# Kernel tuning notes

Measured on AMD Instinct MI355X. Metric: run time of the kernel, lower is better.

The kernel has to match this reference:

```python
import jax, jax.numpy as jnp
import numpy as np

N_NODES = 50000
N_EDGES = 600000
N_FEAT = 128
NHID = 128
N_CLASSES = 10
N_GRAPHS = 512
BN_EPS = 1e-5


def _gcn_conv(x, W, b, src, dst, n):
    """PyG GCNConv: D^{-1/2}(A+I)D^{-1/2} X W + b (symmetric norm, self-loops)."""
    xw = x @ W  # [n, out]
    deg = jax.ops.segment_sum(jnp.ones(src.shape[0], x.dtype), dst, num_segments=n) + 1.0
    dinv = jax.lax.rsqrt(deg)  # [n]
    norm = dinv[src] * dinv[dst]  # [E]
    agg = jax.ops.segment_sum(xw[src] * norm[:, None], dst, num_segments=n)
    agg = agg + xw * (dinv * dinv)[:, None]  # self-loop contribution
    return agg + b


def setup_inputs() -> dict:
    key = jax.random.key(0)
    ks = jax.random.split(key, 16)
    s_in = 1.0 / np.sqrt(N_FEAT)
    s_h = 1.0 / np.sqrt(NHID)
    s_h2 = 1.0 / np.sqrt(NHID // 2)
    return {
        "x": jax.random.normal(ks[0], (N_NODES, N_FEAT), jnp.float32),
        "edge_index": jax.random.randint(ks[1], (2, N_EDGES), 0, N_NODES, jnp.int32),
        "batch": jnp.sort(jax.random.randint(ks[2], (N_NODES,), 0, N_GRAPHS, jnp.int32)),
        "W1": jax.random.normal(ks[3], (N_FEAT, NHID), jnp.float32) * s_in,
        "b1": jnp.zeros((NHID,), jnp.float32),
        "W2": jax.random.normal(ks[4], (NHID, NHID), jnp.float32) * s_h,
        "b2": jnp.zeros((NHID,), jnp.float32),
        "W3": jax.random.normal(ks[5], (NHID, NHID), jnp.float32) * s_h,
        "b3": jnp.zeros((NHID,), jnp.float32),
        "gamma": jnp.ones((NHID,), jnp.float32),
        "beta": jnp.zeros((NHID,), jnp.float32),
        "run_mean": jnp.zeros((NHID,), jnp.float32),
        "run_var": jnp.ones((NHID,), jnp.float32),
        "lw1": jax.random.normal(ks[6], (NHID, NHID), jnp.float32) * s_h,
        "lb1": jnp.zeros((NHID,), jnp.float32),
        "lw2": jax.random.normal(ks[7], (NHID, NHID // 2), jnp.float32) * s_h,
        "lb2": jnp.zeros((NHID // 2,), jnp.float32),
        "lw3": jax.random.normal(ks[8], (NHID // 2, N_CLASSES), jnp.float32) * s_h2,
        "lb3": jnp.zeros((N_CLASSES,), jnp.float32),
    }


def reference(x, edge_index, batch, W1, b1, W2, b2, W3, b3,
              gamma, beta, run_mean, run_var,
              lw1, lb1, lw2, lb2, lw3, lb3):
    src, dst = edge_index[0], edge_index[1]
    h = jax.nn.relu(_gcn_conv(x, W1, b1, src, dst, N_NODES))
    h = jax.nn.relu(_gcn_conv(h, W2, b2, src, dst, N_NODES))
    h = jax.nn.relu(_gcn_conv(h, W3, b3, src, dst, N_NODES))
    # BatchNorm1d (eval: running stats)
    h = (h - run_mean) * jax.lax.rsqrt(run_var + BN_EPS) * gamma + beta
    # scatter_max over graph ids -> [N_GRAPHS, NHID]
    g = jax.ops.segment_max(h, batch, num_segments=N_GRAPHS)
    g = jax.nn.relu(g @ lw1 + lb1)
    g = jax.nn.relu(g @ lw2 + lb2)
    return g @ lw3 + lb3
```

## Files before the change

### kernel.cpp

```cpp
#include <hip/hip_runtime.h>
#include <hip/hip_bf16.h>

#define NHID 128
#define NGRAPH 512
#define NCLS 10

typedef __attribute__((ext_vector_type(8))) short bf16x8;
typedef __attribute__((ext_vector_type(4))) float f32x4;
typedef __attribute__((ext_vector_type(4))) unsigned int u32x4;

__device__ inline unsigned int fenc(float f) {
    unsigned int u = __float_as_uint(f);
    return (u & 0x80000000u) ? ~u : (u | 0x80000000u);
}
__device__ inline float fdec(unsigned int u) {
    u = (u & 0x80000000u) ? (u & 0x7fffffffu) : ~u;
    return __uint_as_float(u);
}
__device__ inline unsigned short f2bf(float f) {
    unsigned int u = __float_as_uint(f);
    return (unsigned short)((u + 0x7fffu + ((u >> 16) & 1u)) >> 16);
}
__device__ inline unsigned int packbf(float lo, float hi) {
    return (unsigned)f2bf(lo) | ((unsigned)f2bf(hi) << 16);
}

__global__ void k_front(const int* __restrict__ dst, int* __restrict__ cnt, int E, int degB,
                        const float* __restrict__ x, unsigned int* __restrict__ xb, int n8, int xB,
                        const float* __restrict__ W1, const float* __restrict__ W2,
                        const float* __restrict__ W3, unsigned short* __restrict__ Wt,
                        unsigned int* __restrict__ keys) {
    int b = blockIdx.x;
    if (b < degB) {
        int e = b * 256 + threadIdx.x;
        if (e < E) atomicAdd(&cnt[dst[e]], 1);
    } else if (b < degB + xB) {
        int i = (b - degB) * 256 + threadIdx.x;
        if (i < n8) {
            const float* p = x + (size_t)i * 8;
            f32x4 a = *reinterpret_cast<const f32x4*>(p);
            f32x4 c = *reinterpret_cast<const f32x4*>(p + 4);
            u32x4 o;
            o[0] = packbf(a[0], a[1]);
            o[1] = packbf(a[2], a[3]);
            o[2] = packbf(c[0], c[1]);
            o[3] = packbf(c[2], c[3]);
            *reinterpret_cast<u32x4*>(xb + (size_t)i * 4) = o;
        }
    } else if (b < degB + xB + 192) {
        int idx = (b - degB - xB) * 256 + threadIdx.x;
        int l = idx >> 14;
        int r = idx & 16383;
        const float* W = (l == 0) ? W1 : (l == 1) ? W2 : W3;
        int c = r & 127, k = r >> 7;
        Wt[l * 16384 + c * NHID + k] = f2bf(W[k * NHID + c]);
    } else {
        int i = (b - degB - xB - 192) * 256 + threadIdx.x;
        if (i < NGRAPH * NHID) keys[i] = 0u;
    }
}

__global__ __launch_bounds__(1024) void k_scan1(const int* __restrict__ cnt,
        float* __restrict__ dinv, int* __restrict__ rowptr,
        int* __restrict__ bsum, int N) {
    __shared__ int lds[1024];
    int t = threadIdx.x;
    int i = blockIdx.x * 1024 + t;
    int v = (i < N) ? cnt[i] : 0;
    if (i < N) dinv[i] = rsqrtf((float)v + 1.0f);
    lds[t] = v;
    __syncthreads();
    for (int off = 1; off < 1024; off <<= 1) {
        int x = (t >= off) ? lds[t - off] : 0;
        __syncthreads();
        lds[t] += x;
        __syncthreads();
    }
    if (i < N) rowptr[i] = lds[t] - v;
    if (t == 1023) bsum[blockIdx.x] = lds[1023];
}

__global__ __launch_bounds__(1024) void k_scan2(int* __restrict__ bsum, int nb) {
    __shared__ int lds[1024];
    int t = threadIdx.x;
    int v = (t < nb) ? bsum[t] : 0;
    lds[t] = v;
    __syncthreads();
    for (int off = 1; off < 1024; off <<= 1) {
        int x = (t >= off) ? lds[t - off] : 0;
        __syncthreads();
        lds[t] += x;
        __syncthreads();
    }
    if (t < nb) bsum[t] = lds[t] - v;
}

__global__ void k_fill(const int* __restrict__ src, const int* __restrict__ dst,
                       const int* __restrict__ rowptr, const int* __restrict__ bsum,
                       int* __restrict__ cursor, int* __restrict__ csr_src, int E) {
    int e = blockIdx.x * blockDim.x + threadIdx.x;
    if (e >= E) return;
    int s = src[e], d = dst[e];
    int pos = rowptr[d] + bsum[d >> 10] + atomicAdd(&cursor[d], 1);
    csr_src[pos] = s;
}

__device__ inline void fma8(const u32x4& u, float nw, float* a) {
#pragma unroll
    for (int q = 0; q < 4; ++q) {
        a[2 * q]     = fmaf(nw, __uint_as_float(u[q] << 16), a[2 * q]);
        a[2 * q + 1] = fmaf(nw, __uint_as_float(u[q] & 0xffff0000u), a[2 * q + 1]);
    }
}

__device__ inline void gather_row(const unsigned int* __restrict__ Hin,
        const int* __restrict__ csr_src, const int* __restrict__ rowptr,
        const int* __restrict__ bsum, const int* __restrict__ cnt,
        const float* __restrict__ dinv, unsigned int (*lds)[68],
        int w, int wv, int g, int l16, int N) {
    if (w < N) {
        float diw = dinv[w];
        u32x4 us = reinterpret_cast<const u32x4*>(Hin + (size_t)w * (NHID / 2))[l16];
        float a[8];
#pragma unroll
        for (int e = 0; e < 8; ++e) a[e] = 0.f;
        int beg = rowptr[w] + bsum[w >> 10];
        int deg = cnt[w];
        int end = beg + deg;
        int trips = (deg + 15) >> 4;
        int j = beg + g;
        for (int t = 0; t < trips; ++t, j += 16) {
            int s0 = w, s1 = w, s2 = w, s3 = w;
            if (j < end)      s0 = csr_src[j];
            if (j + 4 < end)  s1 = csr_src[j + 4];
            if (j + 8 < end)  s2 = csr_src[j + 8];
            if (j + 12 < end) s3 = csr_src[j + 12];
            float n0 = (j < end)      ? dinv[s0] * diw : 0.f;
            float n1 = (j + 4 < end)  ? dinv[s1] * diw : 0.f;
            float n2 = (j + 8 < end)  ? dinv[s2] * diw : 0.f;
            float n3 = (j + 12 < end) ? dinv[s3] * diw : 0.f;
            u32x4 u0 = reinterpret_cast<const u32x4*>(Hin + (size_t)s0 * (NHID / 2))[l16];
            u32x4 u1 = reinterpret_cast<const u32x4*>(Hin + (size_t)s1 * (NHID / 2))[l16];
            u32x4 u2 = reinterpret_cast<const u32x4*>(Hin + (size_t)s2 * (NHID / 2))[l16];
            u32x4 u3 = reinterpret_cast<const u32x4*>(Hin + (size_t)s3 * (NHID / 2))[l16];
            fma8(u0, n0, a);
            fma8(u1, n1, a);
            fma8(u2, n2, a);
            fma8(u3, n3, a);
        }
        if (g == 0) fma8(us, diw * diw, a);
#pragma unroll
        for (int e = 0; e < 8; ++e) {
            a[e] += __shfl_xor(a[e], 16);
            a[e] += __shfl_xor(a[e], 32);
        }
        if (g == 0) {
            u32x4 o;
            o[0] = packbf(a[0], a[1]);
            o[1] = packbf(a[2], a[3]);
            o[2] = packbf(a[4], a[5]);
            o[3] = packbf(a[6], a[7]);
            *reinterpret_cast<u32x4*>(&lds[wv][l16 * 4]) = o;
        }
    } else if (g == 0) {
        u32x4 z = {0u, 0u, 0u, 0u};
        *reinterpret_cast<u32x4*>(&lds[wv][l16 * 4]) = z;
    }
}

__global__ __launch_bounds__(1024) void k_agg_gemm(const unsigned int* __restrict__ Hin,
        const int* __restrict__ csr_src, const int* __restrict__ rowptr,
        const int* __restrict__ bsum, const int* __restrict__ cnt,
        const float* __restrict__ dinv, const unsigned short* __restrict__ Wt,
        const float* __restrict__ bias, unsigned short* __restrict__ Hout, int N) {
    __shared__ unsigned int lds[16][68];
    int wv = threadIdx.x >> 6;
    int lane = threadIdx.x & 63;
    int g = lane >> 4;
    int l16 = lane & 15;
    int w = blockIdx.x * 16 + wv;
    gather_row(Hin, csr_src, rowptr, bsum, cnt, dinv, lds, w, wv, g, l16, N);
    __syncthreads();
    if (wv < 8) {
        int lr = l16;
        int kq = g;
        f32x4 acc = {0.f, 0.f, 0.f, 0.f};
#pragma unroll
        for (int kg = 0; kg < 4; ++kg) {
            bf16x8 af = *reinterpret_cast<const bf16x8*>(&lds[lr][kg * 16 + kq * 4]);
            bf16x8 bf = *reinterpret_cast<const bf16x8*>(
                Wt + (size_t)(wv * 16 + lr) * NHID + kg * 32 + kq * 8);
            acc = __builtin_amdgcn_mfma_f32_16x16x32_bf16(af, bf, acc, 0, 0, 0);
        }
        int c = wv * 16 + lr;
        float b = bias[c];
#pragma unroll
        for (int e = 0; e < 4; ++e) {
            int r = blockIdx.x * 16 + kq * 4 + e;
            if (r < N) {
                float v = fmaxf(acc[e] + b, 0.f);
                Hout[(size_t)r * NHID + c] = f2bf(v);
            }
        }
    }
}

__global__ __launch_bounds__(1024) void k_agg_gemm_bn(const unsigned int* __restrict__ Hin,
        const int* __restrict__ csr_src, const int* __restrict__ rowptr,
        const int* __restrict__ bsum, const int* __restrict__ cnt,
        const float* __restrict__ dinv, const unsigned short* __restrict__ Wt,
        const float* __restrict__ bias, const int* __restrict__ batch,
        const float* __restrict__ gamma, const float* __restrict__ beta,
        const float* __restrict__ rmean, const float* __restrict__ rvar,
        unsigned int* __restrict__ keys, int N) {
    __shared__ unsigned int lds[16][68];
    __shared__ unsigned int smax[16][NHID];
    __shared__ int bseg[16];
    int tid = threadIdx.x;
    int wv = tid >> 6;
    int lane = tid & 63;
    int g = lane >> 4;
    int l16 = lane & 15;
    int n0 = blockIdx.x * 16;
    for (int i = tid; i < 16 * NHID; i += 1024) ((unsigned int*)smax)[i] = 0u;
    if (tid < 16) {
        int r = n0 + tid;
        bseg[tid] = batch[r < N ? r : N - 1];
    }
    int w = n0 + wv;
    gather_row(Hin, csr_src, rowptr, bsum, cnt, dinv, lds, w, wv, g, l16, N);
    __syncthreads();
    if (wv < 8) {
        int lr = l16;
        int kq = g;
        f32x4 acc = {0.f, 0.f, 0.f, 0.f};
#pragma unroll
        for (int kg = 0; kg < 4; ++kg) {
            bf16x8 af = *reinterpret_cast<const bf16x8*>(&lds[lr][kg * 16 + kq * 4]);
            bf16x8 bf = *reinterpret_cast<const bf16x8*>(
                Wt + (size_t)(wv * 16 + lr) * NHID + kg * 32 + kq * 8);
            acc = __builtin_amdgcn_mfma_f32_16x16x32_bf16(af, bf, acc, 0, 0, 0);
        }
        int c = wv * 16 + lr;
        float b = bias[c];
        float sc = gamma[c] * rsqrtf(rvar[c] + 1e-5f);
        float sh = beta[c] - rmean[c] * sc;
        int glo = bseg[0];
#pragma unroll
        for (int e = 0; e < 4; ++e) {
            int rr = kq * 4 + e;
            if (n0 + rr < N) {
                float v = fmaxf(acc[e] + b, 0.f);
                float y = fmaf(v, sc, sh);
                atomicMax(&smax[bseg[rr] - glo][c], fenc(y));
            }
        }
    }
    __syncthreads();
    int glo = bseg[0];
    int last = N - 1 - n0;
    if (last > 15) last = 15;
    int span = bseg[last] - glo + 1;
    for (int i = tid; i < span * NHID; i += 1024) {
        unsigned int v = ((unsigned int*)smax)[i];
        if (v) atomicMax(&keys[(size_t)(glo + (i >> 7)) * NHID + (i & 127)], v);
    }
}

__global__ __launch_bounds__(128) void k_head(const unsigned int* __restrict__ keys,
        const float* __restrict__ lw1, const float* __restrict__ lb1,
        const float* __restrict__ lw2, const float* __restrict__ lb2,
        const float* __restrict__ lw3, const float* __restrict__ lb3,
        float* __restrict__ out) {
    __shared__ float g0[NHID], g1[NHID], g2[64];
    int r = blockIdx.x;
    int t = threadIdx.x;
    unsigned int u = keys[(size_t)r * NHID + t];
    g0[t] = (u == 0u) ? -3.0e38f : fdec(u);
    __syncthreads();
    float acc = lb1[t];
#pragma unroll 8
    for (int k = 0; k < NHID; ++k) acc = fmaf(g0[k], lw1[k * NHID + t], acc);
    g1[t] = fmaxf(acc, 0.f);
    __syncthreads();
    if (t < 64) {
        acc = lb2[t];
#pragma unroll 8
        for (int k = 0; k < NHID; ++k) acc = fmaf(g1[k], lw2[k * 64 + t], acc);
        g2[t] = fmaxf(acc, 0.f);
    }
    __syncthreads();
    if (t < NCLS) {
        acc = lb3[t];
#pragma unroll 8
        for (int k = 0; k < 64; ++k) acc = fmaf(g2[k], lw3[k * NCLS + t], acc);
        out[(size_t)r * NCLS + t] = acc;
    }
}

extern "C" void kernel_launch(void* const* d_in, const int* in_sizes, int n_in,
                              void* d_out, int out_size, void* d_ws, size_t ws_size,
                              hipStream_t stream) {
    const float* x     = (const float*)d_in[0];
    const int*   ei    = (const int*)d_in[1];
    const int*   batch = (const int*)d_in[2];
    const float* W1 = (const float*)d_in[3];
    const float* b1 = (const float*)d_in[4];
    const float* W2 = (const float*)d_in[5];
    const float* b2 = (const float*)d_in[6];
    const float* W3 = (const float*)d_in[7];
    const float* b3 = (const float*)d_in[8];
    const float* gamma = (const float*)d_in[9];
    const float* beta  = (const float*)d_in[10];
    const float* rmean = (const float*)d_in[11];
    const float* rvar  = (const float*)d_in[12];
    const float* lw1 = (const float*)d_in[13];
    const float* lb1 = (const float*)d_in[14];
    const float* lw2 = (const float*)d_in[15];
    const float* lb2 = (const float*)d_in[16];
    const float* lw3 = (const float*)d_in[17];
    const float* lb3 = (const float*)d_in[18];

    const int N = in_sizes[2];
    const int E = in_sizes[1] / 2;
    const int* src = ei;
    const int* dst = ei + E;

    char* ws = (char*)d_ws;
    size_t off = 0;
    auto alloc = [&](size_t bytes) {
        char* p = ws + off;
        off += (bytes + 255) & ~(size_t)255;
        return p;
    };
    int*   cnt     = (int*)  alloc((size_t)N * 8);
    int*   cursor  = cnt + N;
    int*   rowptr  = (int*)  alloc((size_t)N * 4);
    int*   bsum    = (int*)  alloc(1024 * 4);
    float* dinv    = (float*)alloc((size_t)N * 4);
    int*   csr_src = (int*)  alloc((size_t)E * 4);
    unsigned int* xb   = (unsigned int*)alloc((size_t)N * NHID * 2);
    unsigned int* Hb   = (unsigned int*)alloc((size_t)N * NHID * 2);
    unsigned int* H2   = (unsigned int*)alloc((size_t)N * NHID * 2);
    unsigned short* Wt = (unsigned short*)alloc((size_t)3 * NHID * NHID * 2);
    unsigned int* keys = (unsigned int*)alloc((size_t)NGRAPH * NHID * 4);
    (void)ws_size; (void)n_in; (void)out_size;

    hipMemsetAsync(cnt, 0, (size_t)N * 8, stream);

    int degB = (E + 255) / 256;
    int n8 = N * 16;
    int xB = (n8 + 255) / 256;
    int frontB = degB + xB + 192 + (NGRAPH * NHID + 255) / 256;
    k_front<<<frontB, 256, 0, stream>>>(dst, cnt, E, degB, x, xb, n8, xB,
                                        W1, W2, W3, Wt, keys);
    int nb1 = (N + 1023) / 1024;
    k_scan1<<<nb1, 1024, 0, stream>>>(cnt, dinv, rowptr, bsum, N);
    k_scan2<<<1, 1024, 0, stream>>>(bsum, nb1);
    k_fill<<<degB, 256, 0, stream>>>(src, dst, rowptr, bsum, cursor, csr_src, E);

    int fgb = (N + 15) / 16;
    k_agg_gemm<<<fgb, 1024, 0, stream>>>(xb, csr_src, rowptr, bsum, cnt, dinv,
                                         Wt, b1, (unsigned short*)Hb, N);
    k_agg_gemm<<<fgb, 1024, 0, stream>>>(Hb, csr_src, rowptr, bsum, cnt, dinv,
                                         Wt + 16384, b2, (unsigned short*)H2, N);
    k_agg_gemm_bn<<<fgb, 1024, 0, stream>>>(H2, csr_src, rowptr, bsum, cnt, dinv,
                                            Wt + 32768, b3, batch, gamma, beta,
                                            rmean, rvar, keys, N);

    k_head<<<NGRAPH, 128, 0, stream>>>(keys, lw1, lb1, lw2, lb2, lw3, lb3, (float*)d_out);
}
```

Baseline: 234.0 us.

## Process 32 rows per block so all 16 waves run MFMA after gather

Measured after the change: 232.3 us, median of 2. No clear change (-0.7%).

```diff
diff --git a/kernel.cpp b/kernel.cpp
--- a/kernel.cpp
+++ b/kernel.cpp
@@ -117,7 +117,7 @@
         const int* __restrict__ csr_src, const int* __restrict__ rowptr,
         const int* __restrict__ bsum, const int* __restrict__ cnt,
         const float* __restrict__ dinv, unsigned int (*lds)[68],
-        int w, int wv, int g, int l16, int N) {
+        int w, int row, int g, int l16, int N) {
     if (w < N) {
         float diw = dinv[w];
         u32x4 us = reinterpret_cast<const u32x4*>(Hin + (size_t)w * (NHID / 2))[l16];
@@ -160,11 +160,11 @@
             o[1] = packbf(a[2], a[3]);
             o[2] = packbf(a[4], a[5]);
             o[3] = packbf(a[6], a[7]);
-            *reinterpret_cast<u32x4*>(&lds[wv][l16 * 4]) = o;
+            *reinterpret_cast<u32x4*>(&lds[row][l16 * 4]) = o;
         }
     } else if (g == 0) {
         u32x4 z = {0u, 0u, 0u, 0u};
-        *reinterpret_cast<u32x4*>(&lds[wv][l16 * 4]) = z;
+        *reinterpret_cast<u32x4*>(&lds[row][l16 * 4]) = z;
     }
 }
 
@@ -173,34 +173,36 @@
         const int* __restrict__ bsum, const int* __restrict__ cnt,
         const float* __restrict__ dinv, const unsigned short* __restrict__ Wt,
         const float* __restrict__ bias, unsigned short* __restrict__ Hout, int N) {
-    __shared__ unsigned int lds[16][68];
+    __shared__ unsigned int lds[32][68];
     int wv = threadIdx.x >> 6;
     int lane = threadIdx.x & 63;
     int g = lane >> 4;
     int l16 = lane & 15;
-    int w = blockIdx.x * 16 + wv;
-    gather_row(Hin, csr_src, rowptr, bsum, cnt, dinv, lds, w, wv, g, l16, N);
-    __syncthreads();
-    if (wv < 8) {
-        int lr = l16;
-        int kq = g;
-        f32x4 acc = {0.f, 0.f, 0.f, 0.f};
-#pragma unroll
-        for (int kg = 0; kg < 4; ++kg) {
-            bf16x8 af = *reinterpret_cast<const bf16x8*>(&lds[lr][kg * 16 + kq * 4]);
-            bf16x8 bf = *reinterpret_cast<const bf16x8*>(
-                Wt + (size_t)(wv * 16 + lr) * NHID + kg * 32 + kq * 8);
-            acc = __builtin_amdgcn_mfma_f32_16x16x32_bf16(af, bf, acc, 0, 0, 0);
-        }
-        int c = wv * 16 + lr;
-        float b = bias[c];
-#pragma unroll
-        for (int e = 0; e < 4; ++e) {
-            int r = blockIdx.x * 16 + kq * 4 + e;
-            if (r < N) {
-                float v = fmaxf(acc[e] + b, 0.f);
-                Hout[(size_t)r * NHID + c] = f2bf(v);
-            }
+    int n0 = blockIdx.x * 32;
+    gather_row(Hin, csr_src, rowptr, bsum, cnt, dinv, lds, n0 + 2 * wv,     2 * wv,     g, l16, N);
+    gather_row(Hin, csr_src, rowptr, bsum, cnt, dinv, lds, n0 + 2 * wv + 1, 2 * wv + 1, g, l16, N);
+    __syncthreads();
+    int rh = wv >> 3;
+    int ct = wv & 7;
+    int lr = l16;
+    int kq = g;
+    f32x4 acc = {0.f, 0.f, 0.f, 0.f};
+#pragma unroll
+    for (int kg = 0; kg < 4; ++kg) {
+        bf16x8 af = *reinterpret_cast<const bf16x8*>(&lds[rh * 16 + lr][kg * 16 + kq * 4]);
+        bf16x8 bf = *reinterpret_cast<const bf16x8*>(
+            Wt + (size_t)(ct * 16 + lr) * NHID + kg * 32 + kq * 8);
+        acc = __builtin_amdgcn_mfma_f32_16x16x32_bf16(af, bf, acc, 0, 0, 0);
+    }
+    int c = ct * 16 + lr;
+    float b = bias[c];
+#pragma unroll
+    for (int e = 0; e < 4; ++e) {
+        int rr = rh * 16 + kq * 4 + e;
+        int r = n0 + rr;
+        if (r < N) {
+            float v = fmaxf(acc[e] + b, 0.f);
+            Hout[(size_t)r * NHID + c] = f2bf(v);
         }
     }
 }
@@ -213,53 +215,52 @@
         const float* __restrict__ gamma, const float* __restrict__ beta,
         const float* __restrict__ rmean, const float* __restrict__ rvar,
         unsigned int* __restrict__ keys, int N) {
-    __shared__ unsigned int lds[16][68];
-    __shared__ unsigned int smax[16][NHID];
-    __shared__ int bseg[16];
+    __shared__ unsigned int lds[32][68];
+    __shared__ unsigned int smax[32][NHID];
+    __shared__ int bseg[32];
     int tid = threadIdx.x;
     int wv = tid >> 6;
     int lane = tid & 63;
     int g = lane >> 4;
     int l16 = lane & 15;
-    int n0 = blockIdx.x * 16;
-    for (int i = tid; i < 16 * NHID; i += 1024) ((unsigned int*)smax)[i] = 0u;
-    if (tid < 16) {
+    int n0 = blockIdx.x * 32;
+    for (int i = tid; i < 32 * NHID; i += 1024) ((unsigned int*)smax)[i] = 0u;
+    if (tid < 32) {
         int r = n0 + tid;
         bseg[tid] = batch[r < N ? r : N - 1];
     }
-    int w = n0 + wv;
-    gather_row(Hin, csr_src, rowptr, bsum, cnt, dinv, lds, w, wv, g, l16, N);
-    __syncthreads();
-    if (wv < 8) {
-        int lr = l16;
-        int kq = g;
-        f32x4 acc = {0.f, 0.f, 0.f, 0.f};
-#pragma unroll
-        for (int kg = 0; kg < 4; ++kg) {
-            bf16x8 af = *reinterpret_cast<const bf16x8*>(&lds[lr][kg * 16 + kq * 4]);
-            bf16x8 bf = *reinterpret_cast<const bf16x8*>(
-                Wt + (size_t)(wv * 16 + lr) * NHID + kg * 32 + kq * 8);
-            acc = __builtin_amdgcn_mfma_f32_16x16x32_bf16(af, bf, acc, 0, 0, 0);
-        }
-        int c = wv * 16 + lr;
-        float b = bias[c];
-        float sc = gamma[c] * rsqrtf(rvar[c] + 1e-5f);
-        float sh = beta[c] - rmean[c] * sc;
-        int glo = bseg[0];
-#pragma unroll
-        for (int e = 0; e < 4; ++e) {
-            int rr = kq * 4 + e;
-            if (n0 + rr < N) {
-                float v = fmaxf(acc[e] + b, 0.f);
-                float y = fmaf(v, sc, sh);
-                atomicMax(&smax[bseg[rr] - glo][c], fenc(y));
-            }
-        }
-    }
-    __syncthreads();
+    gather_row(Hin, csr_src, rowptr, bsum, cnt, dinv, lds, n0 + 2 * wv,     2 * wv,     g, l16, N);
+    gather_row(Hin, csr_src, rowptr, bsum, cnt, dinv, lds, n0 + 2 * wv + 1, 2 * wv + 1, g, l16, N);
+    __syncthreads();
+    int rh = wv >> 3;
+    int ct = wv & 7;
+    int lr = l16;
+    int kq = g;
+    f32x4 acc = {0.f, 0.f, 0.f, 0.f};
+#pragma unroll
+    for (int kg = 0; kg < 4; ++kg) {
+        bf16x8 af = *reinterpret_cast<const bf16x8*>(&lds[rh * 16 + lr][kg * 16 + kq * 4]);
+        bf16x8 bf = *reinterpret_cast<const bf16x8*>(
+            Wt + (size_t)(ct * 16 + lr) * NHID + kg * 32 + kq * 8);
+        acc = __builtin_amdgcn_mfma_f32_16x16x32_bf16(af, bf, acc, 0, 0, 0);
+    }
+    int c = ct * 16 + lr;
+    float b = bias[c];
+    float sc = gamma[c] * rsqrtf(rvar[c] + 1e-5f);
+    float sh = beta[c] - rmean[c] * sc;
     int glo = bseg[0];
+#pragma unroll
+    for (int e = 0; e < 4; ++e) {
+        int rr = rh * 16 + kq * 4 + e;
+        if (n0 + rr < N) {
+            float v = fmaxf(acc[e] + b, 0.f);
+            float y = fmaf(v, sc, sh);
+            atomicMax(&smax[bseg[rr] - glo][c], fenc(y));
+        }
+    }
+    __syncthreads();
     int last = N - 1 - n0;
-    if (last > 15) last = 15;
+    if (last > 31) last = 31;
     int span = bseg[last] - glo + 1;
     for (int i = tid; i < span * NHID; i += 1024) {
         unsigned int v = ((unsigned int*)smax)[i];
@@ -359,7 +360,7 @@
     k_scan2<<<1, 1024, 0, stream>>>(bsum, nb1);
     k_fill<<<degB, 256, 0, stream>>>(src, dst, rowptr, bsum, cursor, csr_src, E);
 
-    int fgb = (N + 15) / 16;
+    int fgb = (N + 31) / 32;
     k_agg_gemm<<<fgb, 1024, 0, stream>>>(xb, csr_src, rowptr, bsum, cnt, dinv,
                                          Wt, b1, (unsigned short*)Hb, N);
     k_agg_gemm<<<fgb, 1024, 0, stream>>>(Hb, csr_src, rowptr, bsum, cnt, dinv,
```
